# Kernel optimization log

Hardware: AMD Instinct MI355X
Metric: run time of the kernel (lower is better)

The kernel has to match this reference:

```python
import jax, jax.numpy as jnp
import numpy as np

B, C, H = 8, 768, 12
TH = TW = 16
SH = SW = 32
N = TH * TW + SH * SW  # 1280


def setup_inputs() -> dict:
    key = jax.random.key(0)
    k1, k2, k3 = jax.random.split(key, 3)
    return {
        "x": jax.random.normal(k1, (B, N, C), jnp.float32),
        "qkv_w": jax.random.normal(k2, (3 * C, C), jnp.float32) * 0.02,
        "proj_w": jax.random.normal(k3, (C, C), jnp.float32) * 0.02,
        "proj_b": jnp.zeros((C,), jnp.float32),
        "t_h": TH, "t_w": TW, "s_h": SH, "s_w": SW,
    }


def reference(x, qkv_w, proj_w, proj_b, t_h, t_w, s_h, s_w):
    Bb, Nn, Cc = x.shape
    hd = Cc // H
    scale = hd ** -0.5
    nt = t_h * t_w
    ns = s_h * s_w
    # qkv projection: torch Linear computes x @ W.T
    qkv = (x @ qkv_w.T).reshape(Bb, Nn, 3, H, hd).transpose(2, 0, 3, 1, 4)
    q, k, v = qkv[0], qkv[1], qkv[2]  # each [B, H, N, hd]
    q_mt, q_s = q[:, :, :nt], q[:, :, nt:]
    k_mt, v_mt = k[:, :, :nt], v[:, :, :nt]
    # template queries attend only to template keys
    attn_t = jax.nn.softmax(jnp.einsum('bhqd,bhkd->bhqk', q_mt, k_mt) * scale, axis=-1)
    x_mt = jnp.einsum('bhqk,bhkd->bhqd', attn_t, v_mt).transpose(0, 2, 1, 3).reshape(Bb, nt, Cc)
    # search queries attend to all (template + search) keys
    attn_s = jax.nn.softmax(jnp.einsum('bhqd,bhkd->bhqk', q_s, k) * scale, axis=-1)
    x_s = jnp.einsum('bhqk,bhkd->bhqd', attn_s, v).transpose(0, 2, 1, 3).reshape(Bb, ns, Cc)
    out = jnp.concatenate([x_mt, x_s], axis=1)
    out = out @ proj_w.T + proj_b
    return out
```

## Files before the change

### kernel.cpp

```cpp
#include <hip/hip_runtime.h>
#include <hip/hip_bf16.h>


typedef __attribute__((ext_vector_type(8))) short s8v;
typedef __attribute__((ext_vector_type(4))) float f4v;
typedef __attribute__((ext_vector_type(4))) unsigned short u4v;
typedef __attribute__((ext_vector_type(4))) unsigned int u4i;
typedef __attribute__((ext_vector_type(2))) unsigned int u2i;

#define MFMA16(a, b, c) __builtin_amdgcn_mfma_f32_16x16x32_bf16((a), (b), (c), 0, 0, 0)

#define QSCALE 0.1803368801f

__device__ __forceinline__ unsigned short f2bf(float f) {
  unsigned int u = __builtin_bit_cast(unsigned int, f);
  u += 0x7fffu + ((u >> 16) & 1u);
  return (unsigned short)(u >> 16);
}

__device__ __forceinline__ unsigned int pk2(float lo, float hi) {
  __hip_bfloat162 t = __float22bfloat162_rn(make_float2(lo, hi));
  unsigned int u;
  __builtin_memcpy(&u, &t, 4);
  return u;
}

__device__ __forceinline__ s8v pack8(const float* p0, const float* p1) {
  u4i pi;
  pi[0] = pk2(p0[0], p0[1]);
  pi[1] = pk2(p0[2], p0[3]);
  pi[2] = pk2(p1[0], p1[1]);
  pi[3] = pk2(p1[2], p1[3]);
  return __builtin_bit_cast(s8v, pi);
}

__global__ __launch_bounds__(256) void cvt3_kernel(const float* __restrict__ x,
                                                   const float* __restrict__ wq,
                                                   const float* __restrict__ wp,
                                                   unsigned short* __restrict__ xb,
                                                   unsigned short* __restrict__ wqb,
                                                   unsigned short* __restrict__ wpb) {
  int i = blockIdx.x * 256 + threadIdx.x;
  const float* src;
  unsigned short* dst;
  int j;
  if (i < 1966080) {
    src = x; dst = xb; j = i;
  } else if (i < 1966080 + 442368) {
    src = wq; dst = wqb; j = i - 1966080;
  } else {
    src = wp; dst = wpb; j = i - (1966080 + 442368);
  }
  f4v v = ((const f4v*)src)[j];
  u4v o;
  o[0] = f2bf(v[0]); o[1] = f2bf(v[1]); o[2] = f2bf(v[2]); o[3] = f2bf(v[3]);
  ((u4v*)dst)[j] = o;
}


#define GEMM_STAGE(AS, BS, kt_)                                                             \
  do {                                                                                      \
    __builtin_amdgcn_global_load_lds(                                                       \
        (const __attribute__((address_space(1))) unsigned int*)(gA0 + (kt_)),               \
        (__attribute__((address_space(3))) unsigned int*)((char*)(AS) + tid * 16), 16, 0, 0); \
    __builtin_amdgcn_global_load_lds(                                                       \
        (const __attribute__((address_space(1))) unsigned int*)(gA1 + (kt_)),               \
        (__attribute__((address_space(3))) unsigned int*)((char*)(AS) + (512 + tid) * 16),  \
        16, 0, 0);                                                                          \
    __builtin_amdgcn_global_load_lds(                                                       \
        (const __attribute__((address_space(1))) unsigned int*)(gB0 + (kt_)),               \
        (__attribute__((address_space(3))) unsigned int*)((char*)(BS) + tid * 16), 16, 0, 0); \
  } while (0)

#define PIPE_WAIT3(cond_more)                                                               \
  do {                                                                                      \
    if (cond_more) asm volatile("s_waitcnt vmcnt(3) lgkmcnt(0)" ::: "memory");              \
    else           asm volatile("s_waitcnt vmcnt(0) lgkmcnt(0)" ::: "memory");              \
    __builtin_amdgcn_s_barrier();                                                           \
    __builtin_amdgcn_sched_barrier(0);                                                      \
  } while (0)

#define PIPE_WAIT4(cond_more)                                                               \
  do {                                                                                      \
    if (cond_more) asm volatile("s_waitcnt vmcnt(4) lgkmcnt(0)" ::: "memory");              \
    else           asm volatile("s_waitcnt vmcnt(0) lgkmcnt(0)" ::: "memory");              \
    __builtin_amdgcn_s_barrier();                                                           \
    __builtin_amdgcn_sched_barrier(0);                                                      \
  } while (0)

__global__ __launch_bounds__(512) void gemm_qkv_kernel(
    const unsigned short* __restrict__ A,
    const unsigned short* __restrict__ Bm,
    unsigned short* __restrict__ qb, unsigned short* __restrict__ kb,
    unsigned short* __restrict__ vT) {
  const int K = 768;
  __shared__ __align__(16) unsigned short As[3][256 * 32];
  __shared__ __align__(16) unsigned short Bs[3][128 * 32];
  int tid = threadIdx.x;
  int wave = tid >> 6, lane = tid & 63;
  int quad = lane >> 4, l16 = lane & 15;
  int wm = wave >> 1, wn = wave & 1;
  int l = blockIdx.x;
  int xcd = l & 7;
  int idx = l >> 3;
  int by = xcd * 5 + idx / 18;
  int bxg = idx - (idx / 18) * 18;
  int m0 = by * 256, n0 = bxg * 128;

  int srow = tid >> 2;
  int scol = (((tid & 3) ^ ((tid >> 3) & 3)) << 3);
  const unsigned short* gA0 = A + (size_t)(m0 + srow) * K + scol;
  const unsigned short* gA1 = A + (size_t)(m0 + srow + 128) * K + scol;
  const unsigned short* gB0 = Bm + (size_t)(n0 + srow) * K + scol;

  int rquad = quad ^ ((l16 >> 1) & 3);

  f4v acc[4][4];
#pragma unroll
  for (int i = 0; i < 4; ++i)
#pragma unroll
    for (int j = 0; j < 4; ++j) acc[i][j] = (f4v){0.f, 0.f, 0.f, 0.f};

  GEMM_STAGE(As[0], Bs[0], 0);
  GEMM_STAGE(As[1], Bs[1], 32);

  int bfc = 0, bfs = 2;
  for (int t = 0; t < 24; ++t) {
    PIPE_WAIT3(t + 1 < 24);
    if (t + 2 < 24) GEMM_STAGE(As[bfs], Bs[bfs], (t + 2) * 32);

    const unsigned short* Ab = As[bfc];
    const unsigned short* Bb = Bs[bfc];
    s8v af[4], bfr[4];
#pragma unroll
    for (int mi = 0; mi < 4; ++mi)
      af[mi] = *(const s8v*)&Ab[(wm * 64 + mi * 16 + l16) * 32 + rquad * 8];
#pragma unroll
    for (int ni = 0; ni < 4; ++ni)
      bfr[ni] = *(const s8v*)&Bb[(wn * 64 + ni * 16 + l16) * 32 + rquad * 8];
#pragma unroll
    for (int mi = 0; mi < 4; ++mi)
#pragma unroll
      for (int ni = 0; ni < 4; ++ni)
        acc[mi][ni] = MFMA16(af[mi], bfr[ni], acc[mi][ni]);

    bfc = (bfc == 2) ? 0 : bfc + 1;
    bfs = (bfs == 2) ? 0 : bfs + 1;
  }

  int which = n0 / 768;
  if (which == 2) {
#pragma unroll
    for (int ni = 0; ni < 4; ++ni) {
      int oo = n0 + wn * 64 + ni * 16 + l16 - 1536;
      int hh = oo >> 6;
      int dd = oo & 63;
#pragma unroll
      for (int mi = 0; mi < 4; ++mi) {
        int gm = m0 + wm * 64 + mi * 16 + quad * 4;
        int bb = gm / 1280;
        int nn = gm - bb * 1280;
        u2i w;
        w[0] = pk2(acc[mi][ni][0], acc[mi][ni][1]);
        w[1] = pk2(acc[mi][ni][2], acc[mi][ni][3]);
        *(u2i*)(vT + (((size_t)bb * 12 + hh) * 64 + dd) * 1280 + nn) = w;
      }
    }
  } else {
    unsigned short* dst = which ? kb : qb;
    float sc = which ? 1.0f : QSCALE;
#pragma unroll
    for (int ni = 0; ni < 4; ++ni) {
      int oo = n0 + wn * 64 + ni * 16 + l16 - which * 768;
      int hh = oo >> 6;
      int dd = oo & 63;
#pragma unroll
      for (int mi = 0; mi < 4; ++mi) {
#pragma unroll
        for (int r = 0; r < 4; ++r) {
          int gm = m0 + wm * 64 + mi * 16 + quad * 4 + r;
          int bb = gm / 1280;
          int nn = gm - bb * 1280;
          dst[(((size_t)bb * 12 + hh) * 1280 + nn) * 64 + dd] = f2bf(acc[mi][ni][r] * sc);
        }
      }
    }
  }
}

__global__ __launch_bounds__(512) void gemm_proj_kernel(
    const unsigned short* __restrict__ A,
    const unsigned short* __restrict__ Bm,
    const float* __restrict__ pb, float* __restrict__ out) {
  const int K = 768;
  __shared__ __align__(16) unsigned short As[3][256 * 32];
  __shared__ __align__(16) unsigned short Bs[3][128 * 32];
  int tid = threadIdx.x;
  int wave = tid >> 6, lane = tid & 63;
  int quad = lane >> 4, l16 = lane & 15;
  int wm = wave >> 1, wn = wave & 1;
  int l = blockIdx.x;
  int xcd = l & 7;
  int idx = l >> 3;
  int by = xcd * 5 + idx / 6;
  int bxg = idx - (idx / 6) * 6;
  int m0 = by * 256, n0 = bxg * 128;

  int srow = tid >> 2;
  int scol = (((tid & 3) ^ ((tid >> 3) & 3)) << 3);
  const unsigned short* gA0 = A + (size_t)(m0 + srow) * K + scol;
  const unsigned short* gA1 = A + (size_t)(m0 + srow + 128) * K + scol;
  const unsigned short* gB0 = Bm + (size_t)(n0 + srow) * K + scol;

  int rquad = quad ^ ((l16 >> 1) & 3);

  f4v acc[4][4];
#pragma unroll
  for (int i = 0; i < 4; ++i)
#pragma unroll
    for (int j = 0; j < 4; ++j) acc[i][j] = (f4v){0.f, 0.f, 0.f, 0.f};

  GEMM_STAGE(As[0], Bs[0], 0);
  GEMM_STAGE(As[1], Bs[1], 32);

  int bfc = 0, bfs = 2;
  for (int t = 0; t < 24; ++t) {
    PIPE_WAIT3(t + 1 < 24);
    if (t + 2 < 24) GEMM_STAGE(As[bfs], Bs[bfs], (t + 2) * 32);

    const unsigned short* Ab = As[bfc];
    const unsigned short* Bb = Bs[bfc];
    s8v af[4], bfr[4];
#pragma unroll
    for (int mi = 0; mi < 4; ++mi)
      af[mi] = *(const s8v*)&Ab[(wm * 64 + mi * 16 + l16) * 32 + rquad * 8];
#pragma unroll
    for (int ni = 0; ni < 4; ++ni)
      bfr[ni] = *(const s8v*)&Bb[(wn * 64 + ni * 16 + l16) * 32 + rquad * 8];
#pragma unroll
    for (int mi = 0; mi < 4; ++mi)
#pragma unroll
      for (int ni = 0; ni < 4; ++ni)
        acc[mi][ni] = MFMA16(af[mi], bfr[ni], acc[mi][ni]);

    bfc = (bfc == 2) ? 0 : bfc + 1;
    bfs = (bfs == 2) ? 0 : bfs + 1;
  }

#pragma unroll
  for (int ni = 0; ni < 4; ++ni) {
    int gn = n0 + wn * 64 + ni * 16 + l16;
    float bias = pb[gn];
#pragma unroll
    for (int mi = 0; mi < 4; ++mi)
#pragma unroll
      for (int r = 0; r < 4; ++r) {
        int gm = m0 + wm * 64 + mi * 16 + quad * 4 + r;
        out[(size_t)gm * 768 + gn] = acc[mi][ni][r] + bias;
      }
  }
}

__global__ __launch_bounds__(256) void attn_kernel(
    const unsigned short* __restrict__ qb, const unsigned short* __restrict__ kb,
    const unsigned short* __restrict__ vT, unsigned short* __restrict__ attnb) {
  const int NT = 1280, CC = 768;
  int l = blockIdx.x;
  int xcd = l & 7;
  int idx = l >> 3;
  int grp = xcd * 12 + idx / 5;
  int bx = idx - (idx / 5) * 5;
  int b = grp / 12;
  int h = grp - b * 12;
  int nk, qstart;
  if (bx < 4) { nk = 1280; qstart = 256 + bx * 256; }
  else        { nk = 256;  qstart = 0; }
  int wave = threadIdx.x >> 6, lane = threadIdx.x & 63;
  int quad = lane >> 4, l16 = lane & 15;
  int qa = qstart + wave * 64;
  int ntiles = nk >> 6;

  const unsigned short* qp = qb + (((size_t)b * 12 + h) * NT + qa) * 64;
  const unsigned short* kp = kb + (((size_t)b * 12 + h) * NT) * 64;
  const unsigned short* vp = vT + (((size_t)b * 12 + h) * 64) * NT;

  __shared__ __align__(16) unsigned short Kl[3][8][512];
  __shared__ __align__(16) unsigned short Vl[3][8][512];

  s8v bq0 = *(const s8v*)(qp + l16 * 64 + quad * 8);
  s8v bq1 = *(const s8v*)(qp + l16 * 64 + 32 + quad * 8);
  s8v bq2 = *(const s8v*)(qp + (16 + l16) * 64 + quad * 8);
  s8v bq3 = *(const s8v*)(qp + (16 + l16) * 64 + 32 + quad * 8);
  s8v bq4 = *(const s8v*)(qp + (32 + l16) * 64 + quad * 8);
  s8v bq5 = *(const s8v*)(qp + (32 + l16) * 64 + 32 + quad * 8);
  s8v bq6 = *(const s8v*)(qp + (48 + l16) * 64 + quad * 8);
  s8v bq7 = *(const s8v*)(qp + (48 + l16) * 64 + 32 + quad * 8);

  int perm = ((l16 >> 2) << 3) + (l16 & 3);
  int f0 = wave * 2, f1 = wave * 2 + 1;
  int koffs0, koffs1, voffs0, voffs1;
  {
    int s = f0 >> 2, dh = (f0 >> 1) & 1, hh = f0 & 1;
    koffs0 = (s * 32 + hh * 4 + perm) * 64 + (dh * 4 + quad) * 8;
    s = f1 >> 2; dh = (f1 >> 1) & 1; hh = f1 & 1;
    koffs1 = (s * 32 + hh * 4 + perm) * 64 + (dh * 4 + quad) * 8;
    int dt = f0 >> 1, sv = f0 & 1;
    voffs0 = (dt * 16 + l16) * NT + sv * 32 + quad * 8;
    dt = f1 >> 1; sv = f1 & 1;
    voffs1 = (dt * 16 + l16) * NT + sv * 32 + quad * 8;
  }

#define STAGE(bfi, k0_)                                                                     \
  do {                                                                                      \
    __builtin_amdgcn_global_load_lds(                                                       \
        (const __attribute__((address_space(1))) unsigned int*)(kp + (size_t)(k0_)*64 +     \
                                                                koffs0),                    \
        (__attribute__((address_space(3))) unsigned int*)((char*)&Kl[bfi][f0][0] +          \
                                                          lane * 16),                       \
        16, 0, 0);                                                                          \
    __builtin_amdgcn_global_load_lds(                                                       \
        (const __attribute__((address_space(1))) unsigned int*)(kp + (size_t)(k0_)*64 +     \
                                                                koffs1),                    \
        (__attribute__((address_space(3))) unsigned int*)((char*)&Kl[bfi][f1][0] +          \
                                                          lane * 16),                       \
        16, 0, 0);                                                                          \
    __builtin_amdgcn_global_load_lds(                                                       \
        (const __attribute__((address_space(1))) unsigned int*)(vp + (size_t)(k0_) +        \
                                                                voffs0),                    \
        (__attribute__((address_space(3))) unsigned int*)((char*)&Vl[bfi][f0][0] +          \
                                                          lane * 16),                       \
        16, 0, 0);                                                                          \
    __builtin_amdgcn_global_load_lds(                                                       \
        (const __attribute__((address_space(1))) unsigned int*)(vp + (size_t)(k0_) +        \
                                                                voffs1),                    \
        (__attribute__((address_space(3))) unsigned int*)((char*)&Vl[bfi][f1][0] +          \
                                                          lane * 16),                       \
        16, 0, 0);                                                                          \
  } while (0)

#define GROUP(bqA, bqB, bqC, bqD, lA, lB, OA, OB)                                           \
  do {                                                                                      \
    f4v s0a = {0.f, 0.f, 0.f, 0.f}, s1a = {0.f, 0.f, 0.f, 0.f};                             \
    f4v s0b = {0.f, 0.f, 0.f, 0.f}, s1b = {0.f, 0.f, 0.f, 0.f};                             \
    s0a = MFMA16(kf[s4 | 0], bqA, s0a);                                                     \
    s0a = MFMA16(kf[s4 | 2], bqB, s0a);                                                     \
    s1a = MFMA16(kf[s4 | 1], bqA, s1a);                                                     \
    s1a = MFMA16(kf[s4 | 3], bqB, s1a);                                                     \
    s0b = MFMA16(kf[s4 | 0], bqC, s0b);                                                     \
    s0b = MFMA16(kf[s4 | 2], bqD, s0b);                                                     \
    s1b = MFMA16(kf[s4 | 1], bqC, s1b);                                                     \
    s1b = MFMA16(kf[s4 | 3], bqD, s1b);                                                     \
    float p0a[4], p1a[4], p0b[4], p1b[4];                                                   \
    _Pragma("unroll") for (int r = 0; r < 4; ++r) {                                         \
      p0a[r] = __builtin_amdgcn_exp2f(s0a[r]);                                              \
      p1a[r] = __builtin_amdgcn_exp2f(s1a[r]);                                              \
      p0b[r] = __builtin_amdgcn_exp2f(s0b[r]);                                              \
      p1b[r] = __builtin_amdgcn_exp2f(s1b[r]);                                              \
    }                                                                                       \
    lA += ((p0a[0] + p0a[1]) + (p0a[2] + p0a[3])) +                                         \
          ((p1a[0] + p1a[1]) + (p1a[2] + p1a[3]));                                          \
    lB += ((p0b[0] + p0b[1]) + (p0b[2] + p0b[3])) +                                         \
          ((p1b[0] + p1b[1]) + (p1b[2] + p1b[3]));                                          \
    s8v pa = pack8(p0a, p1a);                                                               \
    s8v pbv = pack8(p0b, p1b);                                                              \
    _Pragma("unroll") for (int dt = 0; dt < 4; ++dt) {                                      \
      OA[dt] = MFMA16(vf[dt], pa, OA[dt]);                                                  \
      OB[dt] = MFMA16(vf[dt], pbv, OB[dt]);                                                 \
    }                                                                                       \
  } while (0)

  float la = 0.f, lb = 0.f, lc = 0.f, ld = 0.f;
  f4v Oa[4], Ob[4], Oc[4], Od[4];
#pragma unroll
  for (int dt = 0; dt < 4; ++dt) {
    Oa[dt] = (f4v){0.f, 0.f, 0.f, 0.f};
    Ob[dt] = (f4v){0.f, 0.f, 0.f, 0.f};
    Oc[dt] = (f4v){0.f, 0.f, 0.f, 0.f};
    Od[dt] = (f4v){0.f, 0.f, 0.f, 0.f};
  }

  STAGE(0, 0);
  STAGE(1, 64);

  int bfc = 0, bfs = 2;
  for (int t = 0; t < ntiles; ++t) {
    PIPE_WAIT4(t + 1 < ntiles);
    if (t + 2 < ntiles) STAGE(bfs, (t + 2) * 64);

    s8v kf[8];
#pragma unroll
    for (int ff = 0; ff < 8; ++ff) kf[ff] = *(const s8v*)&Kl[bfc][ff][lane * 8];

#pragma unroll
    for (int s = 0; s < 2; ++s) {
      int s4 = s << 2;
      s8v vf[4];
#pragma unroll
      for (int dt = 0; dt < 4; ++dt) vf[dt] = *(const s8v*)&Vl[bfc][dt * 2 + s][lane * 8];
      GROUP(bq0, bq1, bq2, bq3, la, lb, Oa, Ob);
      GROUP(bq4, bq5, bq6, bq7, lc, ld, Oc, Od);
    }

    bfc = (bfc == 2) ? 0 : bfc + 1;
    bfs = (bfs == 2) ? 0 : bfs + 1;
  }
#undef STAGE
#undef GROUP

  la += __shfl_xor(la, 16, 64);
  la += __shfl_xor(la, 32, 64);
  lb += __shfl_xor(lb, 16, 64);
  lb += __shfl_xor(lb, 32, 64);
  lc += __shfl_xor(lc, 16, 64);
  lc += __shfl_xor(lc, 32, 64);
  ld += __shfl_xor(ld, 16, 64);
  ld += __shfl_xor(ld, 32, 64);
  float inva = 1.f / la, invb = 1.f / lb, invc = 1.f / lc, invd = 1.f / ld;

  size_t rowa = ((size_t)b * NT + qa + l16) * CC + h * 64;
  size_t rowb = ((size_t)b * NT + qa + 16 + l16) * CC + h * 64;
  size_t rowc = ((size_t)b * NT + qa + 32 + l16) * CC + h * 64;
  size_t rowd = ((size_t)b * NT + qa + 48 + l16) * CC + h * 64;
#pragma unroll
  for (int dt = 0; dt < 4; ++dt) {
    u4v ova, ovb, ovc, ovd;
#pragma unroll
    for (int r = 0; r < 4; ++r) {
      ova[r] = f2bf(Oa[dt][r] * inva);
      ovb[r] = f2bf(Ob[dt][r] * invb);
      ovc[r] = f2bf(Oc[dt][r] * invc);
      ovd[r] = f2bf(Od[dt][r] * invd);
    }
    *(u4v*)(attnb + rowa + dt * 16 + quad * 4) = ova;
    *(u4v*)(attnb + rowb + dt * 16 + quad * 4) = ovb;
    *(u4v*)(attnb + rowc + dt * 16 + quad * 4) = ovc;
    *(u4v*)(attnb + rowd + dt * 16 + quad * 4) = ovd;
  }
}

extern "C" void kernel_launch(void* const* d_in, const int* in_sizes, int n_in,
                              void* d_out, int out_size, void* d_ws, size_t ws_size,
                              hipStream_t stream) {
  const float* x = (const float*)d_in[0];
  const float* qkv_w = (const float*)d_in[1];
  const float* proj_w = (const float*)d_in[2];
  const float* proj_b = (const float*)d_in[3];
  float* out = (float*)d_out;

  char* ws = (char*)d_ws;
  unsigned short* xb = (unsigned short*)(ws + 0);
  unsigned short* wqkvb = (unsigned short*)(ws + 15728640);
  unsigned short* wpb = (unsigned short*)(ws + 19267584);
  unsigned short* qb = (unsigned short*)(ws + 20447232);
  unsigned short* kbuf = (unsigned short*)(ws + 36175872);
  unsigned short* vT = (unsigned short*)(ws + 51904512);
  unsigned short* attnb = xb;

  cvt3_kernel<<<dim3(9984), 256, 0, stream>>>(x, qkv_w, proj_w, xb, wqkvb, wpb);

  gemm_qkv_kernel<<<dim3(720), 512, 0, stream>>>(xb, wqkvb, qb, kbuf, vT);
  attn_kernel<<<dim3(480), 256, 0, stream>>>(qb, kbuf, vT, attnb);
  gemm_proj_kernel<<<dim3(240), 512, 0, stream>>>(attnb, wpb, proj_b, out);
}
```

Baseline: 234.5 us.

## Split attention blocks into 2-wave blocks with double-buffered K/V staging

The attention kernel now launches 960 blocks of 128 threads (2 waves, 128 queries each) instead of 480 blocks of 256 threads. Each wave stages four K and four V fragments per tile. The K/V LDS ring drops from triple to double buffering, with a full vmcnt(0) drain and barrier each iteration. This aims to raise block count and occupancy and cut the load imbalance between short template blocks and long search blocks, at the cost of loading K/V twice as often per query and less prefetch depth.

```diff
diff --git a/kernel.cpp b/kernel.cpp
--- a/kernel.cpp
+++ b/kernel.cpp
@@ -80,10 +80,9 @@
     __builtin_amdgcn_sched_barrier(0);                                                      \
   } while (0)
 
-#define PIPE_WAIT4(cond_more)                                                               \
+#define DRAIN_BAR                                                                           \
   do {                                                                                      \
-    if (cond_more) asm volatile("s_waitcnt vmcnt(4) lgkmcnt(0)" ::: "memory");              \
-    else           asm volatile("s_waitcnt vmcnt(0) lgkmcnt(0)" ::: "memory");              \
+    asm volatile("s_waitcnt vmcnt(0) lgkmcnt(0)" ::: "memory");                             \
     __builtin_amdgcn_s_barrier();                                                           \
     __builtin_amdgcn_sched_barrier(0);                                                      \
   } while (0)
@@ -261,20 +260,20 @@
   }
 }
 
-__global__ __launch_bounds__(256) void attn_kernel(
+__global__ __launch_bounds__(128) void attn_kernel(
     const unsigned short* __restrict__ qb, const unsigned short* __restrict__ kb,
     const unsigned short* __restrict__ vT, unsigned short* __restrict__ attnb) {
   const int NT = 1280, CC = 768;
   int l = blockIdx.x;
   int xcd = l & 7;
   int idx = l >> 3;
-  int grp = xcd * 12 + idx / 5;
-  int bx = idx - (idx / 5) * 5;
+  int grp = xcd * 12 + idx / 10;
+  int bx = idx - (idx / 10) * 10;
   int b = grp / 12;
   int h = grp - b * 12;
   int nk, qstart;
-  if (bx < 4) { nk = 1280; qstart = 256 + bx * 256; }
-  else        { nk = 256;  qstart = 0; }
+  if (bx < 8) { nk = 1280; qstart = 256 + bx * 128; }
+  else        { nk = 256;  qstart = (bx - 8) * 128; }
   int wave = threadIdx.x >> 6, lane = threadIdx.x & 63;
   int quad = lane >> 4, l16 = lane & 15;
   int qa = qstart + wave * 64;
@@ -284,8 +283,8 @@
   const unsigned short* kp = kb + (((size_t)b * 12 + h) * NT) * 64;
   const unsigned short* vp = vT + (((size_t)b * 12 + h) * 64) * NT;
 
-  __shared__ __align__(16) unsigned short Kl[3][8][512];
-  __shared__ __align__(16) unsigned short Vl[3][8][512];
+  __shared__ __align__(16) unsigned short Kl[2][8][512];
+  __shared__ __align__(16) unsigned short Vl[2][8][512];
 
   s8v bq0 = *(const s8v*)(qp + l16 * 64 + quad * 8);
   s8v bq1 = *(const s8v*)(qp + l16 * 64 + 32 + quad * 8);
@@ -297,43 +296,68 @@
   s8v bq7 = *(const s8v*)(qp + (48 + l16) * 64 + 32 + quad * 8);
 
   int perm = ((l16 >> 2) << 3) + (l16 & 3);
-  int f0 = wave * 2, f1 = wave * 2 + 1;
-  int koffs0, koffs1, voffs0, voffs1;
+  int f0 = wave * 4, f1 = wave * 4 + 1, f2 = wave * 4 + 2, f3 = wave * 4 + 3;
+  int koffs[4], voffs[4];
   {
-    int s = f0 >> 2, dh = (f0 >> 1) & 1, hh = f0 & 1;
-    koffs0 = (s * 32 + hh * 4 + perm) * 64 + (dh * 4 + quad) * 8;
-    s = f1 >> 2; dh = (f1 >> 1) & 1; hh = f1 & 1;
-    koffs1 = (s * 32 + hh * 4 + perm) * 64 + (dh * 4 + quad) * 8;
-    int dt = f0 >> 1, sv = f0 & 1;
-    voffs0 = (dt * 16 + l16) * NT + sv * 32 + quad * 8;
-    dt = f1 >> 1; sv = f1 & 1;
-    voffs1 = (dt * 16 + l16) * NT + sv * 32 + quad * 8;
+    int fs[4] = {f0, f1, f2, f3};
+#pragma unroll
+    for (int j = 0; j < 4; ++j) {
+      int f = fs[j];
+      int s = f >> 2, dh = (f >> 1) & 1, hh = f & 1;
+      koffs[j] = (s * 32 + hh * 4 + perm) * 64 + (dh * 4 + quad) * 8;
+      int dt = f >> 1, sv = f & 1;
+      voffs[j] = (dt * 16 + l16) * NT + sv * 32 + quad * 8;
+    }
   }
 
 #define STAGE(bfi, k0_)                                                                     \
   do {                                                                                      \
     __builtin_amdgcn_global_load_lds(                                                       \
         (const __attribute__((address_space(1))) unsigned int*)(kp + (size_t)(k0_)*64 +     \
-                                                                koffs0),                    \
+                                                                koffs[0]),                  \
         (__attribute__((address_space(3))) unsigned int*)((char*)&Kl[bfi][f0][0] +          \
                                                           lane * 16),                       \
         16, 0, 0);                                                                          \
     __builtin_amdgcn_global_load_lds(                                                       \
         (const __attribute__((address_space(1))) unsigned int*)(kp + (size_t)(k0_)*64 +     \
-                                                                koffs1),                    \
+                                                                koffs[1]),                  \
         (__attribute__((address_space(3))) unsigned int*)((char*)&Kl[bfi][f1][0] +          \
                                                           lane * 16),                       \
         16, 0, 0);                                                                          \
     __builtin_amdgcn_global_load_lds(                                                       \
+        (const __attribute__((address_space(1))) unsigned int*)(kp + (size_t)(k0_)*64 +     \
+                                                                koffs[2]),                  \
+        (__attribute__((address_space(3))) unsigned int*)((char*)&Kl[bfi][f2][0] +          \
+                                                          lane * 16),                       \
+        16, 0, 0);                                                                          \
+    __builtin_amdgcn_global_load_lds(                                                       \
+        (const __attribute__((address_space(1))) unsigned int*)(kp + (size_t)(k0_)*64 +     \
+                                                                koffs[3]),                  \
+        (__attribute__((address_space(3))) unsigned int*)((char*)&Kl[bfi][f3][0] +          \
+                                                          lane * 16),                       \
+        16, 0, 0);                                                                          \
+    __builtin_amdgcn_global_load_lds(                                                       \
         (const __attribute__((address_space(1))) unsigned int*)(vp + (size_t)(k0_) +        \
-                                                                voffs0),                    \
+                                                                voffs[0]),                  \
         (__attribute__((address_space(3))) unsigned int*)((char*)&Vl[bfi][f0][0] +          \
                                                           lane * 16),                       \
         16, 0, 0);                                                                          \
     __builtin_amdgcn_global_load_lds(                                                       \
         (const __attribute__((address_space(1))) unsigned int*)(vp + (size_t)(k0_) +        \
-                                                                voffs1),                    \
+                                                                voffs[1]),                  \
         (__attribute__((address_space(3))) unsigned int*)((char*)&Vl[bfi][f1][0] +          \
+                                                          lane * 16),                       \
+        16, 0, 0);                                                                          \
+    __builtin_amdgcn_global_load_lds(                                                       \
+        (const __attribute__((address_space(1))) unsigned int*)(vp + (size_t)(k0_) +        \
+                                                                voffs[2]),                  \
+        (__attribute__((address_space(3))) unsigned int*)((char*)&Vl[bfi][f2][0] +          \
+                                                          lane * 16),                       \
+        16, 0, 0);                                                                          \
+    __builtin_amdgcn_global_load_lds(                                                       \
+        (const __attribute__((address_space(1))) unsigned int*)(vp + (size_t)(k0_) +        \
+                                                                voffs[3]),                  \
+        (__attribute__((address_space(3))) unsigned int*)((char*)&Vl[bfi][f3][0] +          \
                                                           lane * 16),                       \
         16, 0, 0);                                                                          \
   } while (0)
@@ -380,29 +404,25 @@
   }
 
   STAGE(0, 0);
-  STAGE(1, 64);
-
-  int bfc = 0, bfs = 2;
+
   for (int t = 0; t < ntiles; ++t) {
-    PIPE_WAIT4(t + 1 < ntiles);
-    if (t + 2 < ntiles) STAGE(bfs, (t + 2) * 64);
+    int bf = t & 1;
+    DRAIN_BAR;
+    if (t + 1 < ntiles) STAGE(bf ^ 1, (t + 1) * 64);
 
     s8v kf[8];
 #pragma unroll
-    for (int ff = 0; ff < 8; ++ff) kf[ff] = *(const s8v*)&Kl[bfc][ff][lane * 8];
+    for (int ff = 0; ff < 8; ++ff) kf[ff] = *(const s8v*)&Kl[bf][ff][lane * 8];
 
 #pragma unroll
     for (int s = 0; s < 2; ++s) {
       int s4 = s << 2;
       s8v vf[4];
 #pragma unroll
-      for (int dt = 0; dt < 4; ++dt) vf[dt] = *(const s8v*)&Vl[bfc][dt * 2 + s][lane * 8];
+      for (int dt = 0; dt < 4; ++dt) vf[dt] = *(const s8v*)&Vl[bf][dt * 2 + s][lane * 8];
       GROUP(bq0, bq1, bq2, bq3, la, lb, Oa, Ob);
       GROUP(bq4, bq5, bq6, bq7, lc, ld, Oc, Od);
     }
-
-    bfc = (bfc == 2) ? 0 : bfc + 1;
-    bfs = (bfs == 2) ? 0 : bfs + 1;
   }
 #undef STAGE
 #undef GROUP
@@ -459,6 +479,6 @@
   cvt3_kernel<<<dim3(9984), 256, 0, stream>>>(x, qkv_w, proj_w, xb, wqkvb, wpb);
 
   gemm_qkv_kernel<<<dim3(720), 512, 0, stream>>>(xb, wqkvb, qb, kbuf, vT);
-  attn_kernel<<<dim3(480), 256, 0, stream>>>(qb, kbuf, vT, attnb);
+  attn_kernel<<<dim3(960), 128, 0, stream>>>(qb, kbuf, vT, attnb);
   gemm_proj_kernel<<<dim3(240), 512, 0, stream>>>(attnb, wpb, proj_b, out);
 }
```

New measurement: 267.1 us. 1.14x slower.
